# Optimization experiments

Measured on AMD Instinct MI355X. Metric: run time of the kernel, lower is better.

The kernel has to match this reference:

```python
import jax, jax.numpy as jnp
import numpy as np

B, S, IN, OUT = 4, 512, 512, 112

def setup_inputs() -> dict:
    key = jax.random.key(0)
    k1, k2, k3, k4 = jax.random.split(key, 4)
    input1 = jax.random.normal(k1, (B, S, IN), dtype=jnp.float32)
    input2 = jax.random.normal(k2, (B, S, IN), dtype=jnp.float32)
    # xavier-uniform-ish init scales
    lim1 = float(np.sqrt(6.0 / (IN + IN)))
    w1 = jax.random.uniform(k3, (IN, OUT, IN), dtype=jnp.float32, minval=-lim1, maxval=lim1)
    lim2 = float(np.sqrt(6.0 / (2 * IN + 1 + OUT)))
    w2 = jax.random.uniform(k4, (2 * IN + 1, OUT), dtype=jnp.float32, minval=-lim2, maxval=lim2)
    return {"input1": input1, "input2": input2, "w1": w1, "w2": w2, "seq_len": S}

def reference(input1, input2, w1, w2, seq_len):
    in_size = input1.shape[-1]
    # Biaffine trilinear term: [B, S, S, OUT]
    logits_1 = jnp.einsum('bxi,ioj,byj->bxyo', input1, w1, input2)
    # Concat-linear term without materializing the [B,S,S,2*IN+1] tensor.
    # Original concatenates (input1 broadcast over y, input1 broadcast over x, ones):
    # note BOTH halves come from input1, faithful to the source code.
    wA = w2[:in_size]          # acts on f1 = input1[b, x]
    wB = w2[in_size:2 * in_size]  # acts on f2 = input1[b, y]
    bias = w2[2 * in_size]     # acts on the appended ones
    termA = jnp.einsum('bxi,io->bxo', input1, wA)  # [B,S,OUT]
    termB = jnp.einsum('byi,io->byo', input1, wB)  # [B,S,OUT]
    logits_2 = termA[:, :, None, :] + termB[:, None, :, :] + bias
    return logits_1 + logits_2
```

## Files before the change

kernel.cpp:

```cpp
#include <hip/hip_runtime.h>
#include <cstdint>

constexpr int B_    = 4;
constexpr int S_    = 512;
constexpr int IN_   = 512;
constexpr int OUT_  = 112;
constexpr int NROW_ = B_ * S_;
constexpr int NN_   = OUT_ * IN_;
constexpr int K_    = IN_;

typedef __attribute__((ext_vector_type(8))) short          s16x8;
typedef __attribute__((ext_vector_type(4))) float          f32x4;
typedef __attribute__((ext_vector_type(8))) unsigned short u16x8;
typedef __attribute__((ext_vector_type(4))) unsigned short u16x4;

__device__ __forceinline__ unsigned short f2bf(float f) {
  union { float f; unsigned u; } v; v.f = f;
  unsigned u = v.u;
  return (unsigned short)((u + 0x7FFFu + ((u >> 16) & 1u)) >> 16);
}

__device__ __forceinline__ void gld_lds16(const void* g, void* l) {
  __builtin_amdgcn_global_load_lds(
      (const __attribute__((address_space(1))) unsigned int*)(unsigned long long)g,
      (__attribute__((address_space(3))) unsigned int*)(unsigned int)(unsigned long long)l,
      16, 0, 0);
}

__global__ __launch_bounds__(256) void cast_kernel(
    const float* __restrict__ in1, const float* __restrict__ in2,
    unsigned short* __restrict__ in1b, unsigned short* __restrict__ in2b) {
  int idx = blockIdx.x * 256 + threadIdx.x;
  float4 v1 = ((const float4*)in1)[idx];
  float4 v2 = ((const float4*)in2)[idx];
  ((u16x4*)in1b)[idx] = (u16x4){f2bf(v1.x), f2bf(v1.y), f2bf(v1.z), f2bf(v1.w)};
  ((u16x4*)in2b)[idx] = (u16x4){f2bf(v2.x), f2bf(v2.y), f2bf(v2.z), f2bf(v2.w)};
}

__global__ __launch_bounds__(256) void transpose_w1(
    const float* __restrict__ w1, unsigned short* __restrict__ w1T) {
  __shared__ unsigned short tile[64][40];
  const int t  = threadIdx.x;
  const int n0 = blockIdx.x * 64;
  const int i0 = blockIdx.y * 32;
#pragma unroll
  for (int p = 0; p < 8; ++p) {
    int il = p * 4 + (t >> 6);
    int nl = t & 63;
    tile[nl][il] = f2bf(w1[(size_t)(i0 + il) * NN_ + n0 + nl]);
  }
  __syncthreads();
  int nl = t >> 2, ch = t & 3;
  u16x8 v = *(const u16x8*)&tile[nl][ch * 8];
  *(u16x8*)&w1T[(size_t)(n0 + nl) * K_ + i0 + ch * 8] = v;
}

__global__ __launch_bounds__(128) void term_kernel(
    const float* __restrict__ in1, const float* __restrict__ w2,
    float* __restrict__ termA, float* __restrict__ termB) {
  const int bx = blockIdx.x;
  const int o  = threadIdx.x;
  if (o >= OUT_) return;
  const float* row = in1 + (size_t)bx * IN_;
  float a = 0.f, c = 0.f;
  for (int i = 0; i < IN_; ++i) {
    float v = row[i];
    a += v * w2[i * OUT_ + o];
    c += v * w2[(IN_ + i) * OUT_ + o];
  }
  termA[bx * OUT_ + o] = a + w2[2 * IN_ * OUT_ + o];
  termB[bx * OUT_ + o] = c;
}

__global__ __launch_bounds__(256) void gemm1_kernel(
    const unsigned short* __restrict__ A,
    const unsigned short* __restrict__ Bm,
    unsigned short* __restrict__ U) {
  __shared__ unsigned short As[2][128 * 32];
  __shared__ unsigned short Bs[2][128 * 32];
  const int tid = threadIdx.x;
  const int wid = tid >> 6, lane = tid & 63;
  const int wm = wid & 1, wn = wid >> 1;

  const int d   = blockIdx.x;
  const int xcd = d & 7, kk = d >> 3;
  const int pan = xcd * 56 + (kk >> 4);
  const int mi  = kk & 15;
  const int m0  = mi * 128;
  const int n0  = pan * 128;

  const int rl0 = wid * 16 + (lane >> 2);
  const int rl1 = rl0 + 64;
  const int kcol = lane & 3;

  const unsigned short* aP0 = A + (size_t)(m0 + rl0) * K_ + kcol * 8;
  const unsigned short* aP1 = A + (size_t)(m0 + rl1) * K_ + kcol * 8;
  const unsigned short* bP0 = Bm + (size_t)(n0 + rl0) * K_ + kcol * 8;
  const unsigned short* bP1 = Bm + (size_t)(n0 + rl1) * K_ + kcol * 8;
  const int la0 = rl0 * 32 + kcol * 8;
  const int la1 = rl1 * 32 + kcol * 8;

  const int ln = lane & 15, q = lane >> 4;
  f32x4 acc[4][4];
#pragma unroll
  for (int i = 0; i < 4; ++i)
#pragma unroll
    for (int j = 0; j < 4; ++j) acc[i][j] = (f32x4){0.f, 0.f, 0.f, 0.f};

  auto stage = [&](int bb) {
    gld_lds16(aP0, &As[bb][la0]); gld_lds16(aP1, &As[bb][la1]);
    gld_lds16(bP0, &Bs[bb][la0]); gld_lds16(bP1, &Bs[bb][la1]);
    aP0 += 32; aP1 += 32; bP0 += 32; bP1 += 32;
  };

  constexpr int NT = K_ / 32;
  stage(0);
  for (int kt = 0; kt < NT; ++kt) {
    const int cur = kt & 1;
    if (kt < NT - 1) {
      stage(cur ^ 1);
      asm volatile("s_waitcnt vmcnt(4)" ::: "memory");
    } else {
      asm volatile("s_waitcnt vmcnt(0)" ::: "memory");
    }
    __builtin_amdgcn_s_barrier();
    s16x8 af[4], bfr[4];
#pragma unroll
    for (int mf = 0; mf < 4; ++mf)
      af[mf] = *(const s16x8*)&As[cur][(wm * 64 + mf * 16 + ln) * 32 + q * 8];
#pragma unroll
    for (int nf = 0; nf < 4; ++nf)
      bfr[nf] = *(const s16x8*)&Bs[cur][(wn * 64 + nf * 16 + ln) * 32 + q * 8];
    asm volatile("s_waitcnt lgkmcnt(0)" ::: "memory");
    __builtin_amdgcn_s_barrier();
#pragma unroll
    for (int mf = 0; mf < 4; ++mf)
#pragma unroll
      for (int nf = 0; nf < 4; ++nf)
        acc[mf][nf] = __builtin_amdgcn_mfma_f32_16x16x32_bf16(af[mf], bfr[nf], acc[mf][nf], 0, 0, 0);
  }
#pragma unroll
  for (int mf = 0; mf < 4; ++mf) {
    const int mrow = m0 + wm * 64 + mf * 16 + q * 4;
#pragma unroll
    for (int nf = 0; nf < 4; ++nf) {
      const int ncol = n0 + wn * 64 + nf * 16 + ln;
#pragma unroll
      for (int r = 0; r < 4; ++r)
        U[(size_t)(mrow + r) * NN_ + ncol] = f2bf(acc[mf][nf][r]);
    }
  }
}

__global__ __launch_bounds__(256) void gemm2_kernel(
    const unsigned short* __restrict__ A,
    const unsigned short* __restrict__ U,
    const float* __restrict__ termA,
    const float* __restrict__ termB,
    float* __restrict__ out) {
  __shared__ unsigned short As[2][128 * 32];
  __shared__ unsigned short Bs[2][128 * 32];
  const int tid = threadIdx.x;
  const int wid = tid >> 6, lane = tid & 63;
  const int wm = wid & 1, wn = wid >> 1;

  const int d   = blockIdx.x;
  const int xcd = d & 7, kk = d >> 3;
  const int pan = xcd * 224 + (kk >> 2);
  const int mi  = kk & 3;
  const int b   = pan / 448;
  const int ni  = pan - b * 448;
  const int m0  = mi * 128;
  const int n0  = ni * 128;

  const int rl0 = wid * 16 + (lane >> 2);
  const int rl1 = rl0 + 64;
  const int kcol = lane & 3;

  const unsigned short* aP0 = A + (size_t)(b * S_ + m0 + rl0) * K_ + kcol * 8;
  const unsigned short* aP1 = A + (size_t)(b * S_ + m0 + rl1) * K_ + kcol * 8;
  const int r2 = n0 + rl0, x0r = r2 / OUT_, o0r = r2 - x0r * OUT_;
  const int r3 = n0 + rl1, x1r = r3 / OUT_, o1r = r3 - x1r * OUT_;
  const unsigned short* bP0 = U + (size_t)(b * S_ + x0r) * NN_ + o0r * K_ + kcol * 8;
  const unsigned short* bP1 = U + (size_t)(b * S_ + x1r) * NN_ + o1r * K_ + kcol * 8;
  const int la0 = rl0 * 32 + kcol * 8;
  const int la1 = rl1 * 32 + kcol * 8;

  const int ln = lane & 15, q = lane >> 4;
  f32x4 acc[4][4];
#pragma unroll
  for (int i = 0; i < 4; ++i)
#pragma unroll
    for (int j = 0; j < 4; ++j) acc[i][j] = (f32x4){0.f, 0.f, 0.f, 0.f};

  auto stage = [&](int bb) {
    gld_lds16(aP0, &As[bb][la0]); gld_lds16(aP1, &As[bb][la1]);
    gld_lds16(bP0, &Bs[bb][la0]); gld_lds16(bP1, &Bs[bb][la1]);
    aP0 += 32; aP1 += 32; bP0 += 32; bP1 += 32;
  };

  constexpr int NT = K_ / 32;
  stage(0);
  for (int kt = 0; kt < NT; ++kt) {
    const int cur = kt & 1;
    if (kt < NT - 1) {
      stage(cur ^ 1);
      asm volatile("s_waitcnt vmcnt(4)" ::: "memory");
    } else {
      asm volatile("s_waitcnt vmcnt(0)" ::: "memory");
    }
    __builtin_amdgcn_s_barrier();
    s16x8 af[4], bfr[4];
#pragma unroll
    for (int mf = 0; mf < 4; ++mf)
      af[mf] = *(const s16x8*)&As[cur][(wm * 64 + mf * 16 + ln) * 32 + q * 8];
#pragma unroll
    for (int nf = 0; nf < 4; ++nf)
      bfr[nf] = *(const s16x8*)&Bs[cur][(wn * 64 + nf * 16 + ln) * 32 + q * 8];
    asm volatile("s_waitcnt lgkmcnt(0)" ::: "memory");
    __builtin_amdgcn_s_barrier();
#pragma unroll
    for (int mf = 0; mf < 4; ++mf)
#pragma unroll
      for (int nf = 0; nf < 4; ++nf)
        acc[mf][nf] = __builtin_amdgcn_mfma_f32_16x16x32_bf16(af[mf], bfr[nf], acc[mf][nf], 0, 0, 0);
  }

#pragma unroll
  for (int nf = 0; nf < 4; ++nf) {
    const int n = n0 + wn * 64 + nf * 16 + ln;
    const int x = n / OUT_, o = n - x * OUT_;
    const float tA = termA[b * NN_ + n];
    const float* tB = termB + b * NN_ + o;
    float* op = out + ((size_t)(b * S_ + x) * S_) * OUT_ + o;
#pragma unroll
    for (int mf = 0; mf < 4; ++mf) {
      const int y0 = m0 + wm * 64 + mf * 16 + q * 4;
#pragma unroll
      for (int r = 0; r < 4; ++r) {
        const int y = y0 + r;
        op[(size_t)y * OUT_] = acc[mf][nf][r] + tA + tB[y * OUT_];
      }
    }
  }
}

extern "C" void kernel_launch(void* const* d_in, const int* in_sizes, int n_in,
                              void* d_out, int out_size, void* d_ws, size_t ws_size,
                              hipStream_t stream) {
  const float* in1 = (const float*)d_in[0];
  const float* in2 = (const float*)d_in[1];
  const float* w1  = (const float*)d_in[2];
  const float* w2  = (const float*)d_in[3];
  float* out = (float*)d_out;

  char* ws = (char*)d_ws;
  size_t off = 0;
  unsigned short* w1T  = (unsigned short*)(ws + off); off += (size_t)NN_ * K_ * 2;
  unsigned short* U    = (unsigned short*)(ws + off); off += (size_t)NROW_ * NN_ * 2;
  unsigned short* in1b = (unsigned short*)(ws + off); off += (size_t)NROW_ * IN_ * 2;
  unsigned short* in2b = (unsigned short*)(ws + off); off += (size_t)NROW_ * IN_ * 2;
  float* termA = (float*)(ws + off); off += (size_t)NROW_ * OUT_ * 4;
  float* termB = (float*)(ws + off); off += (size_t)NROW_ * OUT_ * 4;
  if (ws_size < off) return;

  cast_kernel<<<(NROW_ * IN_ / 4) / 256, 256, 0, stream>>>(in1, in2, in1b, in2b);
  transpose_w1<<<dim3(NN_ / 64, K_ / 32), 256, 0, stream>>>(w1, w1T);
  term_kernel<<<NROW_, 128, 0, stream>>>(in1, w2, termA, termB);
  gemm1_kernel<<<7168, 256, 0, stream>>>(in1b, w1T, U);
  gemm2_kernel<<<7168, 256, 0, stream>>>(in2b, U, termA, termB, out);
}
```

Measured before the change: 1.016 ms.

## Enlarge GEMM tiles to 256x256x64 with swizzled LDS and 8 waves

Both bf16 GEMMs move from 128x128 tiles with K-step 32 and 4 waves to 256x256 tiles with K-step 64 and 8 waves per block. Each wave now holds 8x4 MFMA accumulators. The LDS layout is XOR-swizzled on 16-byte chunks to avoid bank conflicts, and the K loop is fully unrolled. The goal is higher arithmetic intensity and less global and LDS traffic per FLOP. In exchange, LDS use rises to 128KB per block and register pressure grows, which may cut occupancy or cause spills.

```diff
diff --git a/kernel.cpp b/kernel.cpp
--- a/kernel.cpp
+++ b/kernel.cpp
@@ -72,76 +72,90 @@
   termB[bx * OUT_ + o] = c;
 }
 
-__global__ __launch_bounds__(256) void gemm1_kernel(
+
+__global__ __launch_bounds__(512, 2) void gemm1_kernel(
     const unsigned short* __restrict__ A,
     const unsigned short* __restrict__ Bm,
     unsigned short* __restrict__ U) {
-  __shared__ unsigned short As[2][128 * 32];
-  __shared__ unsigned short Bs[2][128 * 32];
-  const int tid = threadIdx.x;
-  const int wid = tid >> 6, lane = tid & 63;
-  const int wm = wid & 1, wn = wid >> 1;
+  __shared__ unsigned short As[2][256 * 64];
+  __shared__ unsigned short Bs[2][256 * 64];
+  const int t = threadIdx.x;
+  const int wid = t >> 6, lane = t & 63;
+  const int wm = wid >> 2, wn = wid & 3;
 
   const int d   = blockIdx.x;
   const int xcd = d & 7, kk = d >> 3;
-  const int pan = xcd * 56 + (kk >> 4);
-  const int mi  = kk & 15;
-  const int m0  = mi * 128;
-  const int n0  = pan * 128;
-
-  const int rl0 = wid * 16 + (lane >> 2);
-  const int rl1 = rl0 + 64;
-  const int kcol = lane & 3;
-
-  const unsigned short* aP0 = A + (size_t)(m0 + rl0) * K_ + kcol * 8;
-  const unsigned short* aP1 = A + (size_t)(m0 + rl1) * K_ + kcol * 8;
-  const unsigned short* bP0 = Bm + (size_t)(n0 + rl0) * K_ + kcol * 8;
-  const unsigned short* bP1 = Bm + (size_t)(n0 + rl1) * K_ + kcol * 8;
-  const int la0 = rl0 * 32 + kcol * 8;
-  const int la1 = rl1 * 32 + kcol * 8;
+  const int pan = xcd * 28 + (kk >> 3);
+  const int mi  = kk & 7;
+  const int m0  = mi * 256;
+  const int n0  = pan * 256;
+
+  const int srow = t >> 3;
+  const int scx  = (t & 7) ^ (srow & 7);
+  const unsigned short* aP[4];
+  const unsigned short* bP[4];
+#pragma unroll
+  for (int l = 0; l < 4; ++l) {
+    aP[l] = A  + (size_t)(m0 + l * 64 + srow) * K_ + scx * 8;
+    bP[l] = Bm + (size_t)(n0 + l * 64 + srow) * K_ + scx * 8;
+  }
+
+  auto stage = [&](int bb) {
+#pragma unroll
+    for (int l = 0; l < 4; ++l) gld_lds16(aP[l], &As[bb][l * 4096 + t * 8]);
+#pragma unroll
+    for (int l = 0; l < 4; ++l) gld_lds16(bP[l], &Bs[bb][l * 4096 + t * 8]);
+#pragma unroll
+    for (int l = 0; l < 4; ++l) { aP[l] += 64; bP[l] += 64; }
+  };
 
   const int ln = lane & 15, q = lane >> 4;
-  f32x4 acc[4][4];
-#pragma unroll
-  for (int i = 0; i < 4; ++i)
+  f32x4 acc[8][4];
+#pragma unroll
+  for (int i = 0; i < 8; ++i)
 #pragma unroll
     for (int j = 0; j < 4; ++j) acc[i][j] = (f32x4){0.f, 0.f, 0.f, 0.f};
 
-  auto stage = [&](int bb) {
-    gld_lds16(aP0, &As[bb][la0]); gld_lds16(aP1, &As[bb][la1]);
-    gld_lds16(bP0, &Bs[bb][la0]); gld_lds16(bP1, &Bs[bb][la1]);
-    aP0 += 32; aP1 += 32; bP0 += 32; bP1 += 32;
-  };
-
-  constexpr int NT = K_ / 32;
+  constexpr int NT = K_ / 64;
   stage(0);
+#pragma unroll
   for (int kt = 0; kt < NT; ++kt) {
     const int cur = kt & 1;
     if (kt < NT - 1) {
       stage(cur ^ 1);
-      asm volatile("s_waitcnt vmcnt(4)" ::: "memory");
+      asm volatile("s_waitcnt vmcnt(8)" ::: "memory");
     } else {
       asm volatile("s_waitcnt vmcnt(0)" ::: "memory");
     }
     __builtin_amdgcn_s_barrier();
-    s16x8 af[4], bfr[4];
-#pragma unroll
-    for (int mf = 0; mf < 4; ++mf)
-      af[mf] = *(const s16x8*)&As[cur][(wm * 64 + mf * 16 + ln) * 32 + q * 8];
-#pragma unroll
-    for (int nf = 0; nf < 4; ++nf)
-      bfr[nf] = *(const s16x8*)&Bs[cur][(wn * 64 + nf * 16 + ln) * 32 + q * 8];
+#pragma unroll
+    for (int ks = 0; ks < 2; ++ks) {
+      s16x8 af[8], bfr[4];
+#pragma unroll
+      for (int mf = 0; mf < 8; ++mf) {
+        const int row = wm * 128 + mf * 16 + ln;
+        const int pc  = ((ks * 4 + q) ^ (ln & 7));
+        af[mf] = *(const s16x8*)&As[cur][row * 64 + pc * 8];
+      }
+#pragma unroll
+      for (int nf = 0; nf < 4; ++nf) {
+        const int row = wn * 64 + nf * 16 + ln;
+        const int pc  = ((ks * 4 + q) ^ (ln & 7));
+        bfr[nf] = *(const s16x8*)&Bs[cur][row * 64 + pc * 8];
+      }
+#pragma unroll
+      for (int mf = 0; mf < 8; ++mf)
+#pragma unroll
+        for (int nf = 0; nf < 4; ++nf)
+          acc[mf][nf] = __builtin_amdgcn_mfma_f32_16x16x32_bf16(af[mf], bfr[nf], acc[mf][nf], 0, 0, 0);
+    }
     asm volatile("s_waitcnt lgkmcnt(0)" ::: "memory");
     __builtin_amdgcn_s_barrier();
-#pragma unroll
-    for (int mf = 0; mf < 4; ++mf)
-#pragma unroll
-      for (int nf = 0; nf < 4; ++nf)
-        acc[mf][nf] = __builtin_amdgcn_mfma_f32_16x16x32_bf16(af[mf], bfr[nf], acc[mf][nf], 0, 0, 0);
-  }
-#pragma unroll
-  for (int mf = 0; mf < 4; ++mf) {
-    const int mrow = m0 + wm * 64 + mf * 16 + q * 4;
+  }
+
+#pragma unroll
+  for (int mf = 0; mf < 8; ++mf) {
+    const int mrow = m0 + wm * 128 + mf * 16 + q * 4;
 #pragma unroll
     for (int nf = 0; nf < 4; ++nf) {
       const int ncol = n0 + wn * 64 + nf * 16 + ln;
@@ -152,78 +166,90 @@
   }
 }
 
-__global__ __launch_bounds__(256) void gemm2_kernel(
+__global__ __launch_bounds__(512, 2) void gemm2_kernel(
     const unsigned short* __restrict__ A,
     const unsigned short* __restrict__ U,
     const float* __restrict__ termA,
     const float* __restrict__ termB,
     float* __restrict__ out) {
-  __shared__ unsigned short As[2][128 * 32];
-  __shared__ unsigned short Bs[2][128 * 32];
-  const int tid = threadIdx.x;
-  const int wid = tid >> 6, lane = tid & 63;
-  const int wm = wid & 1, wn = wid >> 1;
+  __shared__ unsigned short As[2][256 * 64];
+  __shared__ unsigned short Bs[2][256 * 64];
+  const int t = threadIdx.x;
+  const int wid = t >> 6, lane = t & 63;
+  const int wm = wid >> 2, wn = wid & 3;
 
   const int d   = blockIdx.x;
   const int xcd = d & 7, kk = d >> 3;
-  const int pan = xcd * 224 + (kk >> 2);
-  const int mi  = kk & 3;
-  const int b   = pan / 448;
-  const int ni  = pan - b * 448;
-  const int m0  = mi * 128;
-  const int n0  = ni * 128;
-
-  const int rl0 = wid * 16 + (lane >> 2);
-  const int rl1 = rl0 + 64;
-  const int kcol = lane & 3;
-
-  const unsigned short* aP0 = A + (size_t)(b * S_ + m0 + rl0) * K_ + kcol * 8;
-  const unsigned short* aP1 = A + (size_t)(b * S_ + m0 + rl1) * K_ + kcol * 8;
-  const int r2 = n0 + rl0, x0r = r2 / OUT_, o0r = r2 - x0r * OUT_;
-  const int r3 = n0 + rl1, x1r = r3 / OUT_, o1r = r3 - x1r * OUT_;
-  const unsigned short* bP0 = U + (size_t)(b * S_ + x0r) * NN_ + o0r * K_ + kcol * 8;
-  const unsigned short* bP1 = U + (size_t)(b * S_ + x1r) * NN_ + o1r * K_ + kcol * 8;
-  const int la0 = rl0 * 32 + kcol * 8;
-  const int la1 = rl1 * 32 + kcol * 8;
+  const int pan = xcd * 112 + (kk >> 1);
+  const int mi  = kk & 1;
+  const int b   = pan / 224;
+  const int ni  = pan - b * 224;
+  const int m0  = mi * 256;
+  const int n0  = ni * 256;
+
+  const int srow = t >> 3;
+  const int scx  = (t & 7) ^ (srow & 7);
+  const unsigned short* aP[4];
+  const unsigned short* bP[4];
+#pragma unroll
+  for (int l = 0; l < 4; ++l) {
+    aP[l] = A + (size_t)(b * S_ + m0 + l * 64 + srow) * K_ + scx * 8;
+    const int n = n0 + l * 64 + srow;
+    const int x = n / OUT_, o = n - x * OUT_;
+    bP[l] = U + (size_t)(b * S_ + x) * NN_ + o * K_ + scx * 8;
+  }
+
+  auto stage = [&](int bb) {
+#pragma unroll
+    for (int l = 0; l < 4; ++l) gld_lds16(aP[l], &As[bb][l * 4096 + t * 8]);
+#pragma unroll
+    for (int l = 0; l < 4; ++l) gld_lds16(bP[l], &Bs[bb][l * 4096 + t * 8]);
+#pragma unroll
+    for (int l = 0; l < 4; ++l) { aP[l] += 64; bP[l] += 64; }
+  };
 
   const int ln = lane & 15, q = lane >> 4;
-  f32x4 acc[4][4];
-#pragma unroll
-  for (int i = 0; i < 4; ++i)
+  f32x4 acc[8][4];
+#pragma unroll
+  for (int i = 0; i < 8; ++i)
 #pragma unroll
     for (int j = 0; j < 4; ++j) acc[i][j] = (f32x4){0.f, 0.f, 0.f, 0.f};
 
-  auto stage = [&](int bb) {
-    gld_lds16(aP0, &As[bb][la0]); gld_lds16(aP1, &As[bb][la1]);
-    gld_lds16(bP0, &Bs[bb][la0]); gld_lds16(bP1, &Bs[bb][la1]);
-    aP0 += 32; aP1 += 32; bP0 += 32; bP1 += 32;
-  };
-
-  constexpr int NT = K_ / 32;
+  constexpr int NT = K_ / 64;
   stage(0);
+#pragma unroll
   for (int kt = 0; kt < NT; ++kt) {
     const int cur = kt & 1;
     if (kt < NT - 1) {
       stage(cur ^ 1);
-      asm volatile("s_waitcnt vmcnt(4)" ::: "memory");
+      asm volatile("s_waitcnt vmcnt(8)" ::: "memory");
     } else {
       asm volatile("s_waitcnt vmcnt(0)" ::: "memory");
     }
     __builtin_amdgcn_s_barrier();
-    s16x8 af[4], bfr[4];
-#pragma unroll
-    for (int mf = 0; mf < 4; ++mf)
-      af[mf] = *(const s16x8*)&As[cur][(wm * 64 + mf * 16 + ln) * 32 + q * 8];
-#pragma unroll
-    for (int nf = 0; nf < 4; ++nf)
-      bfr[nf] = *(const s16x8*)&Bs[cur][(wn * 64 + nf * 16 + ln) * 32 + q * 8];
+#pragma unroll
+    for (int ks = 0; ks < 2; ++ks) {
+      s16x8 af[8], bfr[4];
+#pragma unroll
+      for (int mf = 0; mf < 8; ++mf) {
+        const int row = wm * 128 + mf * 16 + ln;
+        const int pc  = ((ks * 4 + q) ^ (ln & 7));
+        af[mf] = *(const s16x8*)&As[cur][row * 64 + pc * 8];
+      }
+#pragma unroll
+      for (int nf = 0; nf < 4; ++nf) {
+        const int row = wn * 64 + nf * 16 + ln;
+        const int pc  = ((ks * 4 + q) ^ (ln & 7));
+        bfr[nf] = *(const s16x8*)&Bs[cur][row * 64 + pc * 8];
+      }
+#pragma unroll
+      for (int mf = 0; mf < 8; ++mf)
+#pragma unroll
+        for (int nf = 0; nf < 4; ++nf)
+          acc[mf][nf] = __builtin_amdgcn_mfma_f32_16x16x32_bf16(af[mf], bfr[nf], acc[mf][nf], 0, 0, 0);
+    }
     asm volatile("s_waitcnt lgkmcnt(0)" ::: "memory");
     __builtin_amdgcn_s_barrier();
-#pragma unroll
-    for (int mf = 0; mf < 4; ++mf)
-#pragma unroll
-      for (int nf = 0; nf < 4; ++nf)
-        acc[mf][nf] = __builtin_amdgcn_mfma_f32_16x16x32_bf16(af[mf], bfr[nf], acc[mf][nf], 0, 0, 0);
   }
 
 #pragma unroll
@@ -234,8 +260,8 @@
     const float* tB = termB + b * NN_ + o;
     float* op = out + ((size_t)(b * S_ + x) * S_) * OUT_ + o;
 #pragma unroll
-    for (int mf = 0; mf < 4; ++mf) {
-      const int y0 = m0 + wm * 64 + mf * 16 + q * 4;
+    for (int mf = 0; mf < 8; ++mf) {
+      const int y0 = m0 + wm * 128 + mf * 16 + q * 4;
 #pragma unroll
       for (int r = 0; r < 4; ++r) {
         const int y = y0 + r;
@@ -267,6 +293,6 @@
   cast_kernel<<<(NROW_ * IN_ / 4) / 256, 256, 0, stream>>>(in1, in2, in1b, in2b);
   transpose_w1<<<dim3(NN_ / 64, K_ / 32), 256, 0, stream>>>(w1, w1T);
   term_kernel<<<NROW_, 128, 0, stream>>>(in1, w2, termA, termB);
-  gemm1_kernel<<<7168, 256, 0, stream>>>(in1b, w1T, U);
-  gemm2_kernel<<<7168, 256, 0, stream>>>(in2b, U, termA, termB, out);
-}
+  gemm1_kernel<<<1792, 512, 0, stream>>>(in1b, w1T, U);
+  gemm2_kernel<<<1792, 512, 0, stream>>>(in2b, U, termA, termB, out);
+}
```

After: 998.7 us. No clear change (-1.7%).
